# Kernel tuning notes

Hardware: AMD Instinct MI355X
Metric: run time of the kernel (lower is better)

The kernel has to match this reference:

```python
import jax, jax.numpy as jnp
import numpy as np

F = 128; K = 64; SR_CUT = 10.0
NB = 5; NRI = 3; NRA = 2; NRO = 1
N_ATOMS = 10000; N_PAIRS = 320000


def act(x):
    # shifted softplus: softplus(x) - log(2)
    return jax.nn.softplus(x) - jnp.log(2.0).astype(x.dtype)


def residual(x, W1, b1, W2, b2):
    # PhysNet residual: x + dense2(dense1(act(x))) with activation on dense1
    h = act(act(x) @ W1 + b1)
    return x + h @ W2 + b2


def cutoff_fn(D):
    x = D / SR_CUT
    x3 = x * x * x; x4 = x3 * x; x5 = x4 * x
    return jnp.where(x < 1.0, 1.0 - 6.0 * x5 + 15.0 * x4 - 10.0 * x3, 0.0)


def setup_inputs() -> dict:
    key = jax.random.key(0)
    ks = jax.random.split(key, 24)

    def nrm(k, shape, s=0.05):
        return (jax.random.normal(k, shape) * s).astype(jnp.float32)

    inp = {}
    inp["Z"] = jax.random.randint(ks[0], (N_ATOMS,), 1, 95)
    inp["R"] = (jax.random.normal(ks[1], (N_ATOMS, 3)) * 3.0).astype(jnp.float32)
    inp["idx_i"] = jax.random.randint(ks[2], (N_PAIRS,), 0, N_ATOMS)
    inp["idx_j"] = jax.random.randint(ks[3], (N_PAIRS,), 0, N_ATOMS)
    s3 = float(np.sqrt(3.0))
    inp["embeddings"] = jax.random.uniform(ks[4], (95, F), minval=-s3, maxval=s3).astype(jnp.float32)
    inp["rbf_centers"] = jnp.linspace(1.0, float(np.exp(-SR_CUT)), K).astype(jnp.float32)
    width = (0.5 / ((1.0 - float(np.exp(-SR_CUT))) / K)) ** 2
    inp["rbf_widths"] = jnp.full((K,), width, dtype=jnp.float32)
    inp["k2f_W"] = nrm(ks[5], (NB, K, F))
    inp["Wi"] = nrm(ks[6], (NB, F, F)); inp["bi"] = jnp.zeros((NB, F), jnp.float32)
    inp["Wj"] = nrm(ks[7], (NB, F, F)); inp["bj"] = jnp.zeros((NB, F), jnp.float32)
    inp["ri_W1"] = nrm(ks[8], (NB, NRI, F, F)); inp["ri_b1"] = jnp.zeros((NB, NRI, F), jnp.float32)
    inp["ri_W2"] = nrm(ks[9], (NB, NRI, F, F)); inp["ri_b2"] = jnp.zeros((NB, NRI, F), jnp.float32)
    inp["dW"] = nrm(ks[10], (NB, F, F)); inp["db"] = jnp.zeros((NB, F), jnp.float32)
    inp["u"] = jnp.ones((NB, F), jnp.float32)
    inp["ra_W1"] = nrm(ks[11], (NB, NRA, F, F)); inp["ra_b1"] = jnp.zeros((NB, NRA, F), jnp.float32)
    inp["ra_W2"] = nrm(ks[12], (NB, NRA, F, F)); inp["ra_b2"] = jnp.zeros((NB, NRA, F), jnp.float32)
    inp["ro_W1"] = nrm(ks[13], (NB, NRO, F, F)); inp["ro_b1"] = jnp.zeros((NB, NRO, F), jnp.float32)
    inp["ro_W2"] = nrm(ks[14], (NB, NRO, F, F)); inp["ro_b2"] = jnp.zeros((NB, NRO, F), jnp.float32)
    inp["out_W"] = nrm(ks[15], (NB, F, 2))
    inp["Escale"] = jnp.ones((95,), jnp.float32); inp["Eshift"] = jnp.zeros((95,), jnp.float32)
    inp["Qscale"] = jnp.ones((95,), jnp.float32); inp["Qshift"] = jnp.zeros((95,), jnp.float32)
    return inp


def reference(Z, R, idx_i, idx_j, embeddings, rbf_centers, rbf_widths, k2f_W, Wi, bi, Wj, bj,
              ri_W1, ri_b1, ri_W2, ri_b2, dW, db, u, ra_W1, ra_b1, ra_W2, ra_b2,
              ro_W1, ro_b1, ro_W2, ro_b2, out_W, Escale, Eshift, Qscale, Qshift):
    N = R.shape[0]
    # gather-based interatomic distances: gather -> sub -> sumsq -> relu -> sqrt
    dR = R[idx_i] - R[idx_j]                                   # [P,3]
    Dij = jnp.sqrt(jax.nn.relu(jnp.sum(dR * dR, axis=-1)))     # [P]
    # RBF expansion with smooth cutoff
    rbf = cutoff_fn(Dij)[:, None] * jnp.exp(-rbf_widths * (jnp.exp(-Dij)[:, None] - rbf_centers) ** 2)  # [P,K]
    x = embeddings[Z]                                          # [N,F]
    Ea = jnp.zeros((N,), x.dtype)
    Qa = jnp.zeros((N,), x.dtype)
    nhloss = jnp.zeros((), x.dtype)
    last2 = None
    for b in range(NB):
        # --- interaction layer ---
        g = rbf @ k2f_W[b]                                     # [P,F]
        xa = act(x)
        xi = act(xa @ Wi[b] + bi[b])                           # [N,F]
        xj_feat = act(xa @ Wj[b] + bj[b])                      # [N,F]
        msg = g * xj_feat[idx_j]                               # [P,F] gather + modulate
        m = xi + jax.ops.segment_sum(msg, idx_i, num_segments=N)
        for l in range(NRI):
            m = residual(m, ri_W1[b, l], ri_b1[b, l], ri_W2[b, l], ri_b2[b, l])
        m = act(m)
        x = u[b] * x + m @ dW[b] + db[b]
        for l in range(NRA):
            x = residual(x, ra_W1[b, l], ra_b1[b, l], ra_W2[b, l], ra_b2[b, l])
        # --- output block ---
        o = x
        for l in range(NRO):
            o = residual(o, ro_W1[b, l], ro_b1[b, l], ro_W2[b, l], ro_b2[b, l])
        out = act(o) @ out_W[b]                                # [N,2] -> (Ea, Qa)
        Ea = Ea + out[:, 0]
        Qa = Qa + out[:, 1]
        out2 = out * out
        if b > 0:
            nhloss = nhloss + jnp.mean(out2 / (out2 + last2 + 1e-7))
        last2 = out2
    Ea = Escale[Z] * Ea + Eshift[Z]
    Qa = Qscale[Z] * Qa + Qshift[Z]
    return Ea, Qa, Dij, nhloss
```

## Files before the change

### kernel.cpp

```cpp
#include <hip/hip_runtime.h>

typedef __attribute__((ext_vector_type(8))) short bfrag;
typedef __attribute__((ext_vector_type(4))) float ffrag;

__device__ __forceinline__ unsigned short f2b(float f){
  unsigned int u = __float_as_uint(f);
  return (unsigned short)((u + 0x7FFFu + ((u >> 16) & 1u)) >> 16);
}
__device__ __forceinline__ float actf(float v){
  float e = __builtin_amdgcn_exp2f(-fabsf(v)*1.44269504088896341f);
  return fmaxf(v, 0.f) + __builtin_amdgcn_logf(1.f + e)*0.69314718055994531f - 0.69314718055994531f;
}

__global__ __launch_bounds__(256) void k_zero(float* p, int n){
  int i = blockIdx.x*256 + threadIdx.x;
  if (i < n) p[i] = 0.f;
}

__global__ __launch_bounds__(256) void k_dij_count(
    const float* __restrict__ R, const int* __restrict__ idx_i, const int* __restrict__ idx_j,
    float* __restrict__ DijF, float* __restrict__ Dout, int* __restrict__ counts, int P){
  int p = blockIdx.x*256 + threadIdx.x;
  if (p >= P) return;
  int i = idx_i[p], j = idx_j[p];
  float dx = R[i*3+0] - R[j*3+0];
  float dy = R[i*3+1] - R[j*3+1];
  float dz = R[i*3+2] - R[j*3+2];
  float D = sqrtf(fmaxf(dx*dx + dy*dy + dz*dz, 0.f));
  DijF[p] = D;
  Dout[p] = D;
  atomicAdd(&counts[i], 1);
}

__global__ __launch_bounds__(256) void k_scanA(const int* __restrict__ counts,
    int* __restrict__ locEx, int* __restrict__ bsum, int N){
  __shared__ int buf[256];
  int tid = threadIdx.x, idx = blockIdx.x*256 + tid;
  int v = (idx < N) ? counts[idx] : 0;
  buf[tid] = v;
  __syncthreads();
  for (int off = 1; off < 256; off <<= 1){
    int t = (tid >= off) ? buf[tid-off] : 0;
    __syncthreads();
    buf[tid] += t;
    __syncthreads();
  }
  if (idx < N) locEx[idx] = buf[tid] - v;
  if (tid == 255) bsum[blockIdx.x] = buf[255];
}
__global__ __launch_bounds__(64) void k_scanB(int* __restrict__ bsum,
    int* __restrict__ boff, int nb){
  if (threadIdx.x == 0){
    int acc = 0;
    for (int i = 0; i < nb; ++i){ boff[i] = acc; acc += bsum[i]; }
    boff[nb] = acc;
  }
}
__global__ __launch_bounds__(256) void k_scanC(const int* __restrict__ locEx,
    const int* __restrict__ boff, int* __restrict__ starts, int* __restrict__ cursor,
    int N, int nb){
  int idx = blockIdx.x*256 + threadIdx.x;
  if (idx < N){
    int s = locEx[idx] + boff[blockIdx.x];
    starts[idx] = s; cursor[idx] = s;
  }
  if (idx == 0) starts[N] = boff[nb];
}

__global__ __launch_bounds__(256) void k_scatter(const int* __restrict__ idx_i,
    const int* __restrict__ idx_j, const float* __restrict__ DijF,
    int* __restrict__ cursor, int* __restrict__ i_s, int* __restrict__ j_s,
    float* __restrict__ D_s, int P){
  int p = blockIdx.x*256 + threadIdx.x;
  if (p >= P) return;
  int i = idx_i[p];
  int pos = atomicAdd(&cursor[i], 1);
  i_s[pos] = i;
  j_s[pos] = idx_j[p];
  D_s[pos] = DijF[p];
}

__global__ __launch_bounds__(256) void k_rbf(
    const float* __restrict__ D_s, const float* __restrict__ cent, const float* __restrict__ wid,
    unsigned short* __restrict__ rbf_s, int P){
  int gid = blockIdx.x*256 + threadIdx.x;
  if (gid >= P*64) return;
  int t = gid >> 6, k = gid & 63;
  float D = D_s[t];
  float xc = D * 0.1f;
  float cut = 0.f;
  if (xc < 1.f){
    float x3 = xc*xc*xc, x4 = x3*xc, x5 = x4*xc;
    cut = 1.f - 6.f*x5 + 15.f*x4 - 10.f*x3;
  }
  float tt = expf(-D) - cent[k];
  rbf_s[gid] = f2b(cut * expf(-wid[k]*tt*tt));
}

__global__ __launch_bounds__(256) void k_prep(const float* __restrict__ k2f,
    unsigned short* __restrict__ k2fP){
  int gid = blockIdx.x*256 + threadIdx.x;
  if (gid >= 5120) return;
  int l = gid & 63, fr = (gid >> 6) & 15, b = gid >> 10;
  int tile = fr >> 1, kh = fr & 1;
  const float* src = k2f + (size_t)b*64*128;
  int n = tile*16 + (l & 15);
  int kbase = kh*32 + (l >> 4)*8;
  ushort4 o0, o1;
  o0.x = f2b(src[(kbase+0)*128+n]); o0.y = f2b(src[(kbase+1)*128+n]);
  o0.z = f2b(src[(kbase+2)*128+n]); o0.w = f2b(src[(kbase+3)*128+n]);
  o1.x = f2b(src[(kbase+4)*128+n]); o1.y = f2b(src[(kbase+5)*128+n]);
  o1.z = f2b(src[(kbase+6)*128+n]); o1.w = f2b(src[(kbase+7)*128+n]);
  ushort4* dst = (ushort4*)(k2fP + (size_t)gid*8);
  dst[0] = o0; dst[1] = o1;
}

__global__ __launch_bounds__(256) void k_prepAll(
    const float* __restrict__ riW1, const float* __restrict__ riW2,
    const float* __restrict__ dW,   const float* __restrict__ raW1,
    const float* __restrict__ raW2, const float* __restrict__ roW1,
    const float* __restrict__ roW2, const float* __restrict__ Wi,
    const float* __restrict__ Wj,   unsigned short* __restrict__ WBall){
  int gid = blockIdx.x*256 + threadIdx.x;
  if (gid >= 75*2048) return;
  int i = gid >> 11, r = gid & 2047;
  const float* S;
  int slot;
  if (i < 15)      { S = riW1 + (size_t)i*16384;      slot = (i/3)*15 + 2*(i%3); }
  else if (i < 30) { int j=i-15; S = riW2 + (size_t)j*16384; slot = (j/3)*15 + 2*(j%3) + 1; }
  else if (i < 35) { int j=i-30; S = dW   + (size_t)j*16384; slot = j*15 + 6; }
  else if (i < 45) { int j=i-35; S = raW1 + (size_t)j*16384; slot = (j/2)*15 + 7 + 2*(j%2); }
  else if (i < 55) { int j=i-45; S = raW2 + (size_t)j*16384; slot = (j/2)*15 + 8 + 2*(j%2); }
  else if (i < 60) { int j=i-55; S = roW1 + (size_t)j*16384; slot = j*15 + 11; }
  else if (i < 65) { int j=i-60; S = roW2 + (size_t)j*16384; slot = j*15 + 12; }
  else if (i < 70) { int j=i-65; S = Wi   + (size_t)j*16384; slot = ((j==0)?4:(j-1))*15 + 13; }
  else             { int j=i-70; S = Wj   + (size_t)j*16384; slot = ((j==0)?4:(j-1))*15 + 14; }
  int fr = r >> 6, l = r & 63;
  int T = fr >> 2, k0 = fr & 3;
  int n = T*16 + (l & 15);
  int kbase = k0*32 + (l >> 4)*8;
  unsigned short* D = WBall + ((size_t)slot*2048 + r)*8;
  ushort4 o0, o1;
  o0.x=f2b(S[(kbase+0)*128+n]); o0.y=f2b(S[(kbase+1)*128+n]);
  o0.z=f2b(S[(kbase+2)*128+n]); o0.w=f2b(S[(kbase+3)*128+n]);
  o1.x=f2b(S[(kbase+4)*128+n]); o1.y=f2b(S[(kbase+5)*128+n]);
  o1.z=f2b(S[(kbase+6)*128+n]); o1.w=f2b(S[(kbase+7)*128+n]);
  ((ushort4*)D)[0]=o0; ((ushort4*)D)[1]=o1;
}

__global__ __launch_bounds__(256) void k_prepO(const float* __restrict__ outW,
    unsigned short* __restrict__ outWB){
  int gid = blockIdx.x*256 + threadIdx.x;
  if (gid >= 5*256) return;
  int b = gid >> 8, r = gid & 255;
  int l = r & 63;
  int col = l & 15;
  int k0 = r >> 6;
  int kbase = k0*32 + (l >> 4)*8;
  ushort4 o0 = {0,0,0,0}, o1 = {0,0,0,0};
  if (col < 2){
    const float* S = outW + (size_t)b*256;
    o0.x=f2b(S[(kbase+0)*2+col]); o0.y=f2b(S[(kbase+1)*2+col]);
    o0.z=f2b(S[(kbase+2)*2+col]); o0.w=f2b(S[(kbase+3)*2+col]);
    o1.x=f2b(S[(kbase+4)*2+col]); o1.y=f2b(S[(kbase+5)*2+col]);
    o1.z=f2b(S[(kbase+6)*2+col]); o1.w=f2b(S[(kbase+7)*2+col]);
  }
  unsigned short* D = outWB + ((size_t)b*256 + r)*8;
  ((ushort4*)D)[0]=o0; ((ushort4*)D)[1]=o1;
}

__device__ __forceinline__ void mmtile(const unsigned short* tile,
    const unsigned short* __restrict__ WB, int w, int l, ffrag C[4]){
  int m = l & 15, q = l >> 4;
  bfrag A[4];
  #pragma unroll
  for (int k0 = 0; k0 < 4; ++k0)
    A[k0] = *(const bfrag*)(tile + m*136 + k0*32 + q*8);
  #pragma unroll
  for (int tt = 0; tt < 4; ++tt){
    ffrag c = {0.f,0.f,0.f,0.f};
    const bfrag* bp = (const bfrag*)(WB + (((w*4+tt)*4)*64 + l)*8);
    #pragma unroll
    for (int k0 = 0; k0 < 4; ++k0)
      c = __builtin_amdgcn_mfma_f32_16x16x32_bf16(A[k0], bp[k0*64], c, 0, 0, 0);
    C[tt] = c;
  }
}

__device__ __forceinline__ void mmtile2(const unsigned short* tile,
    const unsigned short* __restrict__ WB, int w, int l, ffrag C[2]){
  int m = l & 15, q = l >> 4;
  bfrag A[4];
  #pragma unroll
  for (int k0 = 0; k0 < 4; ++k0)
    A[k0] = *(const bfrag*)(tile + m*136 + k0*32 + q*8);
  #pragma unroll
  for (int tt = 0; tt < 2; ++tt){
    ffrag c = {0.f,0.f,0.f,0.f};
    const bfrag* bp = (const bfrag*)(WB + (((w*2+tt)*4)*64 + l)*8);
    #pragma unroll
    for (int k0 = 0; k0 < 4; ++k0)
      c = __builtin_amdgcn_mfma_f32_16x16x32_bf16(A[k0], bp[k0*64], c, 0, 0, 0);
    C[tt] = c;
  }
}

__global__ __launch_bounds__(128) void k_phase1m(
    const int* __restrict__ Z, const float* __restrict__ emb,
    const unsigned short* __restrict__ WB45,
    const float* __restrict__ bi0, const float* __restrict__ bj0,
    float* __restrict__ x_g, float* __restrict__ m_g, float* __restrict__ xjb_g, int N){
  __shared__ unsigned short tile[16*136];
  int tid = threadIdx.x, w = tid >> 6, l = tid & 63;
  int m = l & 15, q = l >> 4, rbase = blockIdx.x*16;
  #pragma unroll
  for (int r = 0; r < 4; ++r){
    int row = rbase + q*4 + r;
    int z = Z[row];
    #pragma unroll
    for (int tt = 0; tt < 4; ++tt){
      int c = (w*4+tt)*16 + m;
      float v = emb[(size_t)z*128 + c];
      x_g[(size_t)row*128 + c] = v;
      tile[(q*4+r)*136 + c] = f2b(actf(v));
    }
  }
  __syncthreads();
  ffrag C[4];
  mmtile(tile, WB45 + 13*16384, w, l, C);
  #pragma unroll
  for (int tt = 0; tt < 4; ++tt){
    int c = (w*4+tt)*16 + m;
    float bb = bi0[c];
    #pragma unroll
    for (int r = 0; r < 4; ++r)
      m_g[(size_t)(rbase + q*4 + r)*128 + c] = actf(C[tt][r] + bb);
  }
  mmtile(tile, WB45 + 14*16384, w, l, C);
  #pragma unroll
  for (int tt = 0; tt < 4; ++tt){
    int c = (w*4+tt)*16 + m;
    float bb = bj0[c];
    #pragma unroll
    for (int r = 0; r < 4; ++r)
      xjb_g[(size_t)(rbase + q*4 + r)*128 + c] = actf(C[tt][r] + bb);
  }
}

__global__ __launch_bounds__(256) void k_pairmsg2(
    const unsigned short* __restrict__ rbf_s, const unsigned short* __restrict__ k2fP,
    const int* __restrict__ i_s, const int* __restrict__ j_s,
    const float* __restrict__ xj, float* __restrict__ m_g, int P){
  __shared__ float G[4][16*130];
  int tid = threadIdx.x, w = tid >> 6, l = tid & 63;
  float* Gw = &G[w][0];
  bfrag B[8][2];
  #pragma unroll
  for (int t = 0; t < 8; ++t){
    #pragma unroll
    for (int kh = 0; kh < 2; ++kh)
      B[t][kh] = *(const bfrag*)(k2fP + (size_t)((t*2+kh)*64 + l)*8);
  }
  int wstart = (blockIdx.x*4 + w)*128;
  if (wstart >= P) return;
  int row16 = l & 15, quad = l >> 4;
  float a0 = 0.f, a1 = 0.f;
  int iCur = -1;
  #pragma unroll 1
  for (int bt = wstart; bt < wstart + 128; bt += 16){
    int arow = bt + row16;
    bfrag A0 = *(const bfrag*)(rbf_s + (size_t)arow*64 + quad*8);
    bfrag A1 = *(const bfrag*)(rbf_s + (size_t)arow*64 + 32 + quad*8);
    int4 iv[4], jv[4];
    #pragma unroll
    for (int g = 0; g < 4; ++g){
      iv[g] = *(const int4*)(i_s + bt + g*4);
      jv[g] = *(const int4*)(j_s + bt + g*4);
    }
    const int* ip = (const int*)iv;
    const int* jp = (const int*)jv;
    float2 xv[16];
    #pragma unroll
    for (int k = 0; k < 16; ++k)
      xv[k] = *(const float2*)(xj + (size_t)jp[k]*128 + 2*l);
    #pragma unroll
    for (int t = 0; t < 8; ++t){
      ffrag C = {0.f,0.f,0.f,0.f};
      C = __builtin_amdgcn_mfma_f32_16x16x32_bf16(A0, B[t][0], C, 0, 0, 0);
      C = __builtin_amdgcn_mfma_f32_16x16x32_bf16(A1, B[t][1], C, 0, 0, 0);
      #pragma unroll
      for (int r = 0; r < 4; ++r)
        Gw[(quad*4+r)*130 + t*16 + row16] = C[r];
    }
    #pragma unroll
    for (int k = 0; k < 16; ++k){
      int i = ip[k];
      if (i != iCur){
        if (iCur >= 0){
          unsafeAtomicAdd(&m_g[(size_t)iCur*128 + 2*l],     a0);
          unsafeAtomicAdd(&m_g[(size_t)iCur*128 + 2*l + 1], a1);
        }
        iCur = i; a0 = 0.f; a1 = 0.f;
      }
      float g0 = Gw[k*130 + 2*l], g1 = Gw[k*130 + 2*l + 1];
      a0 = fmaf(g0, xv[k].x, a0);
      a1 = fmaf(g1, xv[k].y, a1);
    }
  }
  if (iCur >= 0){
    unsafeAtomicAdd(&m_g[(size_t)iCur*128 + 2*l],     a0);
    unsafeAtomicAdd(&m_g[(size_t)iCur*128 + 2*l + 1], a1);
  }
}

template<int HASNEXT, int NH>
__global__ __launch_bounds__(256) void k_phase2m(
    float* __restrict__ m_g, float* __restrict__ x_g, float* __restrict__ xjb_g,
    const unsigned short* __restrict__ WBb,
    const float* __restrict__ rib1, const float* __restrict__ rib2,
    const float* __restrict__ db, const float* __restrict__ u,
    const float* __restrict__ rab1, const float* __restrict__ rab2,
    const float* __restrict__ rob1, const float* __restrict__ rob2,
    const float* __restrict__ biN, const float* __restrict__ bjN,
    const unsigned short* __restrict__ outWBb,
    float* __restrict__ Ea, float* __restrict__ Qa,
    float* __restrict__ last2, float* __restrict__ nh, int N){
  __shared__ unsigned short tiles[2][16*136];
  __shared__ float biasS[16*128];
  int tid = threadIdx.x, w = tid >> 6, l = tid & 63;
  int m = l & 15, q = l >> 4, rbase = blockIdx.x*16;
  ffrag mC[2], xC[2], C[2];
  int cur = 0;

  if (tid < 128){
    biasS[0*128+tid]  = rib1[tid];
    biasS[1*128+tid]  = rib1[128+tid];
    biasS[2*128+tid]  = rib1[256+tid];
    biasS[3*128+tid]  = rib2[tid];
    biasS[4*128+tid]  = rib2[128+tid];
    biasS[5*128+tid]  = rib2[256+tid];
    biasS[6*128+tid]  = db[tid];
    biasS[7*128+tid]  = u[tid];
    biasS[8*128+tid]  = rab1[tid];
    biasS[9*128+tid]  = rab1[128+tid];
    biasS[10*128+tid] = rab2[tid];
    biasS[11*128+tid] = rab2[128+tid];
    biasS[12*128+tid] = rob1[tid];
    biasS[13*128+tid] = rob2[tid];
    biasS[14*128+tid] = biN[tid];
    biasS[15*128+tid] = bjN[tid];
  }
  #pragma unroll
  for (int tt = 0; tt < 2; ++tt){
    int c = (w*2+tt)*16 + m;
    #pragma unroll
    for (int r = 0; r < 4; ++r){
      float v = m_g[(size_t)(rbase + q*4 + r)*128 + c];
      mC[tt][r] = v;
      tiles[0][(q*4+r)*136 + c] = f2b(actf(v));
    }
  }
  #pragma unroll 1
  for (int li = 0; li < 3; ++li){
    __syncthreads();
    mmtile2(tiles[cur], WBb + (size_t)(2*li)*16384, w, l, C);
    #pragma unroll
    for (int tt = 0; tt < 2; ++tt){
      int c = (w*2+tt)*16 + m;
      float bb = biasS[li*128 + c];
      #pragma unroll
      for (int r = 0; r < 4; ++r)
        tiles[1-cur][(q*4+r)*136 + c] = f2b(actf(C[tt][r] + bb));
    }
    cur ^= 1;
    __syncthreads();
    mmtile2(tiles[cur], WBb + (size_t)(2*li+1)*16384, w, l, C);
    #pragma unroll
    for (int tt = 0; tt < 2; ++tt){
      int c = (w*2+tt)*16 + m;
      float bb = biasS[(3+li)*128 + c];
      #pragma unroll
      for (int r = 0; r < 4; ++r){
        float nv = mC[tt][r] + C[tt][r] + bb;
        mC[tt][r] = nv;
        tiles[1-cur][(q*4+r)*136 + c] = f2b(actf(nv));
      }
    }
    cur ^= 1;
  }
  __syncthreads();
  mmtile2(tiles[cur], WBb + (size_t)6*16384, w, l, C);
  #pragma unroll
  for (int tt = 0; tt < 2; ++tt){
    int c = (w*2+tt)*16 + m;
    float uu = biasS[7*128 + c], bb = biasS[6*128 + c];
    #pragma unroll
    for (int r = 0; r < 4; ++r){
      float xv = x_g[(size_t)(rbase + q*4 + r)*128 + c];
      float nv = uu*xv + C[tt][r] + bb;
      xC[tt][r] = nv;
      tiles[1-cur][(q*4+r)*136 + c] = f2b(actf(nv));
    }
  }
  cur ^= 1;
  #pragma unroll 1
  for (int li = 0; li < 2; ++li){
    __syncthreads();
    mmtile2(tiles[cur], WBb + (size_t)(7+2*li)*16384, w, l, C);
    #pragma unroll
    for (int tt = 0; tt < 2; ++tt){
      int c = (w*2+tt)*16 + m;
      float bb = biasS[(8+li)*128 + c];
      #pragma unroll
      for (int r = 0; r < 4; ++r)
        tiles[1-cur][(q*4+r)*136 + c] = f2b(actf(C[tt][r] + bb));
    }
    cur ^= 1;
    __syncthreads();
    mmtile2(tiles[cur], WBb + (size_t)(8+2*li)*16384, w, l, C);
    #pragma unroll
    for (int tt = 0; tt < 2; ++tt){
      int c = (w*2+tt)*16 + m;
      float bb = biasS[(10+li)*128 + c];
      #pragma unroll
      for (int r = 0; r < 4; ++r){
        float nv = xC[tt][r] + C[tt][r] + bb;
        xC[tt][r] = nv;
        tiles[1-cur][(q*4+r)*136 + c] = f2b(actf(nv));
        if (HASNEXT && li == 1)
          x_g[(size_t)(rbase + q*4 + r)*128 + c] = nv;
      }
    }
    cur ^= 1;
  }
  if (HASNEXT){
    __syncthreads();
    mmtile2(tiles[cur], WBb + (size_t)13*16384, w, l, C);
    #pragma unroll
    for (int tt = 0; tt < 2; ++tt){
      int c = (w*2+tt)*16 + m;
      float bb = biasS[14*128 + c];
      #pragma unroll
      for (int r = 0; r < 4; ++r)
        m_g[(size_t)(rbase + q*4 + r)*128 + c] = actf(C[tt][r] + bb);
    }
    mmtile2(tiles[cur], WBb + (size_t)14*16384, w, l, C);
    #pragma unroll
    for (int tt = 0; tt < 2; ++tt){
      int c = (w*2+tt)*16 + m;
      float bb = biasS[15*128 + c];
      #pragma unroll
      for (int r = 0; r < 4; ++r)
        xjb_g[(size_t)(rbase + q*4 + r)*128 + c] = actf(C[tt][r] + bb);
    }
  }
  __syncthreads();
  mmtile2(tiles[cur], WBb + (size_t)11*16384, w, l, C);
  #pragma unroll
  for (int tt = 0; tt < 2; ++tt){
    int c = (w*2+tt)*16 + m;
    float bb = biasS[12*128 + c];
    #pragma unroll
    for (int r = 0; r < 4; ++r)
      tiles[1-cur][(q*4+r)*136 + c] = f2b(actf(C[tt][r] + bb));
  }
  cur ^= 1;
  __syncthreads();
  mmtile2(tiles[cur], WBb + (size_t)12*16384, w, l, C);
  #pragma unroll
  for (int tt = 0; tt < 2; ++tt){
    int c = (w*2+tt)*16 + m;
    float bb = biasS[13*128 + c];
    #pragma unroll
    for (int r = 0; r < 4; ++r){
      float ov = xC[tt][r] + C[tt][r] + bb;
      tiles[1-cur][(q*4+r)*136 + c] = f2b(actf(ov));
    }
  }
  cur ^= 1;
  __syncthreads();
  if (w == 0){
    bfrag A[4];
    #pragma unroll
    for (int k0 = 0; k0 < 4; ++k0)
      A[k0] = *(const bfrag*)(&tiles[cur][0] + m*136 + k0*32 + q*8);
    ffrag Ch = {0.f,0.f,0.f,0.f};
    #pragma unroll
    for (int k0 = 0; k0 < 4; ++k0){
      bfrag B = *(const bfrag*)(outWBb + (size_t)(k0*64 + l)*8);
      Ch = __builtin_amdgcn_mfma_f32_16x16x32_bf16(A[k0], B, Ch, 0, 0, 0);
    }
    int col = m;
    if (col < 2){
      float tp = 0.f;
      #pragma unroll
      for (int r = 0; r < 4; ++r){
        int row = rbase + q*4 + r;
        float val = Ch[r];
        if (col == 0) Ea[row] += val; else Qa[row] += val;
        float sq = val*val;
        if (NH){
          float lastv = last2[row*2 + col];
          tp += sq/(sq + lastv + 1e-7f);
        }
        last2[row*2 + col] = sq;
      }
      if (NH) unsafeAtomicAdd(nh, tp);
    }
  }
}

__global__ __launch_bounds__(256) void k_final(
    const int* __restrict__ Z, const float* __restrict__ Ea, const float* __restrict__ Qa,
    const float* __restrict__ Es, const float* __restrict__ Eh,
    const float* __restrict__ Qs, const float* __restrict__ Qh,
    const float* __restrict__ nh, float* __restrict__ out, int N, int P){
  int n = blockIdx.x*256 + threadIdx.x;
  if (n < N){
    int z = Z[n];
    out[n]   = Es[z]*Ea[n] + Eh[z];
    out[N+n] = Qs[z]*Qa[n] + Qh[z];
  }
  if (blockIdx.x == 0 && threadIdx.x == 0)
    out[(size_t)2*N + P] = nh[0] / (2.f * (float)N);
}

extern "C" void kernel_launch(void* const* d_in, const int* in_sizes, int n_in,
                              void* d_out, int out_size, void* d_ws, size_t ws_size,
                              hipStream_t stream){
  const int N = in_sizes[0];
  const int P = in_sizes[2];
  const int F = 128;

  const int* Z      = (const int*)d_in[0];
  const float* R    = (const float*)d_in[1];
  const int* idx_i  = (const int*)d_in[2];
  const int* idx_j  = (const int*)d_in[3];
  const float* emb  = (const float*)d_in[4];
  const float* cent = (const float*)d_in[5];
  const float* wid  = (const float*)d_in[6];
  const float* k2f  = (const float*)d_in[7];
  const float* Wi   = (const float*)d_in[8];  const float* bi   = (const float*)d_in[9];
  const float* Wj   = (const float*)d_in[10]; const float* bj   = (const float*)d_in[11];
  const float* riW1 = (const float*)d_in[12]; const float* rib1 = (const float*)d_in[13];
  const float* riW2 = (const float*)d_in[14]; const float* rib2 = (const float*)d_in[15];
  const float* dWp  = (const float*)d_in[16]; const float* dbp  = (const float*)d_in[17];
  const float* u    = (const float*)d_in[18];
  const float* raW1 = (const float*)d_in[19]; const float* rab1 = (const float*)d_in[20];
  const float* raW2 = (const float*)d_in[21]; const float* rab2 = (const float*)d_in[22];
  const float* roW1 = (const float*)d_in[23]; const float* rob1 = (const float*)d_in[24];
  const float* roW2 = (const float*)d_in[25]; const float* rob2 = (const float*)d_in[26];
  const float* outW = (const float*)d_in[27];
  const float* Es   = (const float*)d_in[28]; const float* Eh   = (const float*)d_in[29];
  const float* Qs   = (const float*)d_in[30]; const float* Qh   = (const float*)d_in[31];

  char* ws = (char*)d_ws;
  size_t off = 0;
  float* DijF  = (float*)(ws + off); off += (size_t)P*4;
  float* D_s   = (float*)(ws + off); off += (size_t)P*4;
  int*   i_s   = (int*)  (ws + off); off += (size_t)P*4;
  int*   j_s   = (int*)  (ws + off); off += (size_t)P*4;
  unsigned short* rbf_s = (unsigned short*)(ws + off); off += (size_t)P*64*2;
  unsigned short* k2fP  = (unsigned short*)(ws + off); off += (size_t)5*16*64*8*2;
  unsigned short* WBall = (unsigned short*)(ws + off); off += (size_t)75*16384*2;
  unsigned short* outWB = (unsigned short*)(ws + off); off += (size_t)5*2048*2;
  float* x     = (float*)(ws + off); off += (size_t)N*F*4;
  float* xjb   = (float*)(ws + off); off += (size_t)N*F*4;
  float* m     = (float*)(ws + off); off += (size_t)N*F*4;
  float* last2 = (float*)(ws + off); off += (size_t)N*2*4;
  float* Ea    = (float*)(ws + off); off += (size_t)N*4;
  float* Qa    = (float*)(ws + off); off += (size_t)N*4;
  float* nh    = (float*)(ws + off); off += 256;
  int*   counts= (int*)  (ws + off); off += (size_t)N*4;
  int*   starts= (int*)  (ws + off); off += (size_t)(N+1)*4;
  int*   cursor= (int*)  (ws + off); off += (size_t)N*4;
  int*   locEx = (int*)  (ws + off); off += (size_t)N*4;
  int*   bsum  = (int*)  (ws + off); off += 64*4;
  int*   boff  = (int*)  (ws + off); off += 68*4;

  float* outF = (float*)d_out;
  float* Dout = outF + (size_t)2*N;

  const int nb = (N + 255)/256;
  const int nzero = 3*N + 64;
  k_zero<<<dim3((nzero+255)/256), dim3(256), 0, stream>>>(Ea, nzero);
  k_dij_count<<<dim3((P+255)/256), dim3(256), 0, stream>>>(R, idx_i, idx_j, DijF, Dout, counts, P);
  k_scanA<<<dim3(nb), dim3(256), 0, stream>>>(counts, locEx, bsum, N);
  k_scanB<<<dim3(1), dim3(64), 0, stream>>>(bsum, boff, nb);
  k_scanC<<<dim3(nb), dim3(256), 0, stream>>>(locEx, boff, starts, cursor, N, nb);
  k_scatter<<<dim3((P+255)/256), dim3(256), 0, stream>>>(idx_i, idx_j, DijF, cursor, i_s, j_s, D_s, P);
  k_rbf<<<dim3((P*64+255)/256), dim3(256), 0, stream>>>(D_s, cent, wid, rbf_s, P);
  k_prep<<<dim3(20), dim3(256), 0, stream>>>(k2f, k2fP);
  k_prepAll<<<dim3((75*2048+255)/256), dim3(256), 0, stream>>>(riW1, riW2, dWp, raW1, raW2,
                                                               roW1, roW2, Wi, Wj, WBall);
  k_prepO<<<dim3(5), dim3(256), 0, stream>>>(outW, outWB);

  const int G16 = (N + 15)/16;
  k_phase1m<<<dim3(G16), dim3(128), 0, stream>>>(Z, emb, WBall + (size_t)4*15*16384,
                                                 bi, bj, x, m, xjb, N);

  const int pmg = (P + 511)/512;
  for (int b = 0; b < 5; ++b){
    k_pairmsg2<<<dim3(pmg), dim3(256), 0, stream>>>(rbf_s, k2fP + (size_t)b*16*64*8,
                                                    i_s, j_s, xjb, m, P);
    const unsigned short* WBb = WBall + (size_t)b*15*16384;
    const float* a_rib1 = rib1 + (size_t)b*3*F;
    const float* a_rib2 = rib2 + (size_t)b*3*F;
    const float* a_db   = dbp  + (size_t)b*F;
    const float* a_u    = u    + (size_t)b*F;
    const float* a_rab1 = rab1 + (size_t)b*2*F;
    const float* a_rab2 = rab2 + (size_t)b*2*F;
    const float* a_rob1 = rob1 + (size_t)b*F;
    const float* a_rob2 = rob2 + (size_t)b*F;
    int bn = (b < 4) ? (b+1) : 0;
    const float* a_biN = bi + (size_t)bn*F;
    const float* a_bjN = bj + (size_t)bn*F;
    const unsigned short* oWB = outWB + (size_t)b*2048;
    if (b == 0){
      k_phase2m<1,0><<<dim3(G16), dim3(256), 0, stream>>>(m, x, xjb, WBb,
        a_rib1, a_rib2, a_db, a_u, a_rab1, a_rab2, a_rob1, a_rob2,
        a_biN, a_bjN, oWB, Ea, Qa, last2, nh, N);
    } else if (b < 4){
      k_phase2m<1,1><<<dim3(G16), dim3(256), 0, stream>>>(m, x, xjb, WBb,
        a_rib1, a_rib2, a_db, a_u, a_rab1, a_rab2, a_rob1, a_rob2,
        a_biN, a_bjN, oWB, Ea, Qa, last2, nh, N);
    } else {
      k_phase2m<0,1><<<dim3(G16), dim3(256), 0, stream>>>(m, x, xjb, WBb,
        a_rib1, a_rib2, a_db, a_u, a_rab1, a_rab2, a_rob1, a_rob2,
        a_biN, a_bjN, oWB, Ea, Qa, last2, nh, N);
    }
  }
  k_final<<<dim3((N+255)/256), dim3(256), 0, stream>>>(Z, Ea, Qa, Es, Eh, Qs, Qh, nh, outF, N, P);
}
```

Measured before the change: 520.8 us.

## Software-pipeline weight fragment and rbf/index loads in pair and node kernels

Measured after the change: 518.9 us (median of 2 runs). About the same (-0.4%).

```diff
diff --git a/kernel.cpp b/kernel.cpp
--- a/kernel.cpp
+++ b/kernel.cpp
@@ -187,8 +187,16 @@
   }
 }
 
-__device__ __forceinline__ void mmtile2(const unsigned short* tile,
-    const unsigned short* __restrict__ WB, int w, int l, ffrag C[2]){
+__device__ __forceinline__ void loadB8(const unsigned short* __restrict__ WB,
+    int w, int l, bfrag* B){
+  #pragma unroll
+  for (int tt = 0; tt < 2; ++tt)
+    #pragma unroll
+    for (int k0 = 0; k0 < 4; ++k0)
+      B[tt*4+k0] = *(const bfrag*)(WB + ((size_t)((((w*2+tt)*4)+k0)*64 + l))*8);
+}
+__device__ __forceinline__ void mmB(const unsigned short* tile, const bfrag* B,
+    int l, ffrag C[2]){
   int m = l & 15, q = l >> 4;
   bfrag A[4];
   #pragma unroll
@@ -197,10 +205,9 @@
   #pragma unroll
   for (int tt = 0; tt < 2; ++tt){
     ffrag c = {0.f,0.f,0.f,0.f};
-    const bfrag* bp = (const bfrag*)(WB + (((w*2+tt)*4)*64 + l)*8);
     #pragma unroll
     for (int k0 = 0; k0 < 4; ++k0)
-      c = __builtin_amdgcn_mfma_f32_16x16x32_bf16(A[k0], bp[k0*64], c, 0, 0, 0);
+      c = __builtin_amdgcn_mfma_f32_16x16x32_bf16(A[k0], B[tt*4+k0], c, 0, 0, 0);
     C[tt] = c;
   }
 }
@@ -254,29 +261,29 @@
   __shared__ float G[4][16*130];
   int tid = threadIdx.x, w = tid >> 6, l = tid & 63;
   float* Gw = &G[w][0];
-  bfrag B[8][2];
+  bfrag B[16];
   #pragma unroll
   for (int t = 0; t < 8; ++t){
     #pragma unroll
     for (int kh = 0; kh < 2; ++kh)
-      B[t][kh] = *(const bfrag*)(k2fP + (size_t)((t*2+kh)*64 + l)*8);
+      B[t*2+kh] = *(const bfrag*)(k2fP + (size_t)((t*2+kh)*64 + l)*8);
   }
   int wstart = (blockIdx.x*4 + w)*128;
   if (wstart >= P) return;
   int row16 = l & 15, quad = l >> 4;
   float a0 = 0.f, a1 = 0.f;
   int iCur = -1;
+  bfrag A0 = *(const bfrag*)(rbf_s + (size_t)(wstart + row16)*64 + quad*8);
+  bfrag A1 = *(const bfrag*)(rbf_s + (size_t)(wstart + row16)*64 + 32 + quad*8);
+  int4 iv[4], jv[4];
+  #pragma unroll
+  for (int g = 0; g < 4; ++g){
+    iv[g] = *(const int4*)(i_s + wstart + g*4);
+    jv[g] = *(const int4*)(j_s + wstart + g*4);
+  }
   #pragma unroll 1
-  for (int bt = wstart; bt < wstart + 128; bt += 16){
-    int arow = bt + row16;
-    bfrag A0 = *(const bfrag*)(rbf_s + (size_t)arow*64 + quad*8);
-    bfrag A1 = *(const bfrag*)(rbf_s + (size_t)arow*64 + 32 + quad*8);
-    int4 iv[4], jv[4];
-    #pragma unroll
-    for (int g = 0; g < 4; ++g){
-      iv[g] = *(const int4*)(i_s + bt + g*4);
-      jv[g] = *(const int4*)(j_s + bt + g*4);
-    }
+  for (int bi2 = 0; bi2 < 8; ++bi2){
+    int bt = wstart + bi2*16;
     const int* ip = (const int*)iv;
     const int* jp = (const int*)jv;
     float2 xv[16];
@@ -286,11 +293,23 @@
     #pragma unroll
     for (int t = 0; t < 8; ++t){
       ffrag C = {0.f,0.f,0.f,0.f};
-      C = __builtin_amdgcn_mfma_f32_16x16x32_bf16(A0, B[t][0], C, 0, 0, 0);
-      C = __builtin_amdgcn_mfma_f32_16x16x32_bf16(A1, B[t][1], C, 0, 0, 0);
+      C = __builtin_amdgcn_mfma_f32_16x16x32_bf16(A0, B[t*2],   C, 0, 0, 0);
+      C = __builtin_amdgcn_mfma_f32_16x16x32_bf16(A1, B[t*2+1], C, 0, 0, 0);
       #pragma unroll
       for (int r = 0; r < 4; ++r)
         Gw[(quad*4+r)*130 + t*16 + row16] = C[r];
+    }
+    bfrag nA0, nA1;
+    int4 niv[4], njv[4];
+    if (bi2 < 7){
+      int btn = bt + 16;
+      nA0 = *(const bfrag*)(rbf_s + (size_t)(btn + row16)*64 + quad*8);
+      nA1 = *(const bfrag*)(rbf_s + (size_t)(btn + row16)*64 + 32 + quad*8);
+      #pragma unroll
+      for (int g = 0; g < 4; ++g){
+        niv[g] = *(const int4*)(i_s + btn + g*4);
+        njv[g] = *(const int4*)(j_s + btn + g*4);
+      }
     }
     #pragma unroll
     for (int k = 0; k < 16; ++k){
@@ -305,6 +324,11 @@
       float g0 = Gw[k*130 + 2*l], g1 = Gw[k*130 + 2*l + 1];
       a0 = fmaf(g0, xv[k].x, a0);
       a1 = fmaf(g1, xv[k].y, a1);
+    }
+    if (bi2 < 7){
+      A0 = nA0; A1 = nA1;
+      #pragma unroll
+      for (int g = 0; g < 4; ++g){ iv[g] = niv[g]; jv[g] = njv[g]; }
     }
   }
   if (iCur >= 0){
@@ -331,6 +355,11 @@
   int m = l & 15, q = l >> 4, rbase = blockIdx.x*16;
   ffrag mC[2], xC[2], C[2];
   int cur = 0;
+  const int nst = HASNEXT ? 15 : 13;
+  const int slotSeq[15] = {0,1,2,3,4,5,6,7,8,9,10,
+                           HASNEXT?13:11, HASNEXT?14:12, 11, 12};
+  bfrag Bb[2][8];
+  loadB8(WBb + (size_t)slotSeq[0]*16384, w, l, Bb[0]);
 
   if (tid < 128){
     biasS[0*128+tid]  = rib1[tid];
@@ -350,6 +379,14 @@
     biasS[14*128+tid] = biN[tid];
     biasS[15*128+tid] = bjN[tid];
   }
+  float xrow[2][4];
+  #pragma unroll
+  for (int tt = 0; tt < 2; ++tt){
+    int c = (w*2+tt)*16 + m;
+    #pragma unroll
+    for (int r = 0; r < 4; ++r)
+      xrow[tt][r] = x_g[(size_t)(rbase + q*4 + r)*128 + c];
+  }
   #pragma unroll
   for (int tt = 0; tt < 2; ++tt){
     int c = (w*2+tt)*16 + m;
@@ -360,124 +397,95 @@
       tiles[0][(q*4+r)*136 + c] = f2b(actf(v));
     }
   }
-  #pragma unroll 1
-  for (int li = 0; li < 3; ++li){
+  #pragma unroll
+  for (int s = 0; s < nst; ++s){
     __syncthreads();
-    mmtile2(tiles[cur], WBb + (size_t)(2*li)*16384, w, l, C);
-    #pragma unroll
-    for (int tt = 0; tt < 2; ++tt){
-      int c = (w*2+tt)*16 + m;
-      float bb = biasS[li*128 + c];
-      #pragma unroll
-      for (int r = 0; r < 4; ++r)
-        tiles[1-cur][(q*4+r)*136 + c] = f2b(actf(C[tt][r] + bb));
-    }
-    cur ^= 1;
-    __syncthreads();
-    mmtile2(tiles[cur], WBb + (size_t)(2*li+1)*16384, w, l, C);
-    #pragma unroll
-    for (int tt = 0; tt < 2; ++tt){
-      int c = (w*2+tt)*16 + m;
-      float bb = biasS[(3+li)*128 + c];
-      #pragma unroll
-      for (int r = 0; r < 4; ++r){
-        float nv = mC[tt][r] + C[tt][r] + bb;
-        mC[tt][r] = nv;
-        tiles[1-cur][(q*4+r)*136 + c] = f2b(actf(nv));
-      }
-    }
-    cur ^= 1;
-  }
-  __syncthreads();
-  mmtile2(tiles[cur], WBb + (size_t)6*16384, w, l, C);
-  #pragma unroll
-  for (int tt = 0; tt < 2; ++tt){
-    int c = (w*2+tt)*16 + m;
-    float uu = biasS[7*128 + c], bb = biasS[6*128 + c];
-    #pragma unroll
-    for (int r = 0; r < 4; ++r){
-      float xv = x_g[(size_t)(rbase + q*4 + r)*128 + c];
-      float nv = uu*xv + C[tt][r] + bb;
-      xC[tt][r] = nv;
-      tiles[1-cur][(q*4+r)*136 + c] = f2b(actf(nv));
-    }
-  }
-  cur ^= 1;
-  #pragma unroll 1
-  for (int li = 0; li < 2; ++li){
-    __syncthreads();
-    mmtile2(tiles[cur], WBb + (size_t)(7+2*li)*16384, w, l, C);
-    #pragma unroll
-    for (int tt = 0; tt < 2; ++tt){
-      int c = (w*2+tt)*16 + m;
-      float bb = biasS[(8+li)*128 + c];
-      #pragma unroll
-      for (int r = 0; r < 4; ++r)
-        tiles[1-cur][(q*4+r)*136 + c] = f2b(actf(C[tt][r] + bb));
-    }
-    cur ^= 1;
-    __syncthreads();
-    mmtile2(tiles[cur], WBb + (size_t)(8+2*li)*16384, w, l, C);
-    #pragma unroll
-    for (int tt = 0; tt < 2; ++tt){
-      int c = (w*2+tt)*16 + m;
-      float bb = biasS[(10+li)*128 + c];
-      #pragma unroll
-      for (int r = 0; r < 4; ++r){
-        float nv = xC[tt][r] + C[tt][r] + bb;
-        xC[tt][r] = nv;
-        tiles[1-cur][(q*4+r)*136 + c] = f2b(actf(nv));
-        if (HASNEXT && li == 1)
-          x_g[(size_t)(rbase + q*4 + r)*128 + c] = nv;
-      }
-    }
-    cur ^= 1;
-  }
-  if (HASNEXT){
-    __syncthreads();
-    mmtile2(tiles[cur], WBb + (size_t)13*16384, w, l, C);
-    #pragma unroll
-    for (int tt = 0; tt < 2; ++tt){
-      int c = (w*2+tt)*16 + m;
-      float bb = biasS[14*128 + c];
-      #pragma unroll
-      for (int r = 0; r < 4; ++r)
-        m_g[(size_t)(rbase + q*4 + r)*128 + c] = actf(C[tt][r] + bb);
-    }
-    mmtile2(tiles[cur], WBb + (size_t)14*16384, w, l, C);
-    #pragma unroll
-    for (int tt = 0; tt < 2; ++tt){
-      int c = (w*2+tt)*16 + m;
-      float bb = biasS[15*128 + c];
-      #pragma unroll
-      for (int r = 0; r < 4; ++r)
-        xjb_g[(size_t)(rbase + q*4 + r)*128 + c] = actf(C[tt][r] + bb);
-    }
-  }
-  __syncthreads();
-  mmtile2(tiles[cur], WBb + (size_t)11*16384, w, l, C);
-  #pragma unroll
-  for (int tt = 0; tt < 2; ++tt){
-    int c = (w*2+tt)*16 + m;
-    float bb = biasS[12*128 + c];
-    #pragma unroll
-    for (int r = 0; r < 4; ++r)
-      tiles[1-cur][(q*4+r)*136 + c] = f2b(actf(C[tt][r] + bb));
-  }
-  cur ^= 1;
-  __syncthreads();
-  mmtile2(tiles[cur], WBb + (size_t)12*16384, w, l, C);
-  #pragma unroll
-  for (int tt = 0; tt < 2; ++tt){
-    int c = (w*2+tt)*16 + m;
-    float bb = biasS[13*128 + c];
-    #pragma unroll
-    for (int r = 0; r < 4; ++r){
-      float ov = xC[tt][r] + C[tt][r] + bb;
-      tiles[1-cur][(q*4+r)*136 + c] = f2b(actf(ov));
-    }
-  }
-  cur ^= 1;
+    if (s+1 < nst) loadB8(WBb + (size_t)slotSeq[s+1]*16384, w, l, Bb[(s+1)&1]);
+    mmB(tiles[cur], Bb[s&1], l, C);
+    if (HASNEXT && s == 11){
+      #pragma unroll
+      for (int tt = 0; tt < 2; ++tt){
+        int c = (w*2+tt)*16 + m;
+        float bb = biasS[14*128 + c];
+        #pragma unroll
+        for (int r = 0; r < 4; ++r)
+          m_g[(size_t)(rbase + q*4 + r)*128 + c] = actf(C[tt][r] + bb);
+      }
+    } else if (HASNEXT && s == 12){
+      #pragma unroll
+      for (int tt = 0; tt < 2; ++tt){
+        int c = (w*2+tt)*16 + m;
+        float bb = biasS[15*128 + c];
+        #pragma unroll
+        for (int r = 0; r < 4; ++r)
+          xjb_g[(size_t)(rbase + q*4 + r)*128 + c] = actf(C[tt][r] + bb);
+      }
+    } else if (s == 6){
+      #pragma unroll
+      for (int tt = 0; tt < 2; ++tt){
+        int c = (w*2+tt)*16 + m;
+        float uu = biasS[7*128 + c], bb = biasS[6*128 + c];
+        #pragma unroll
+        for (int r = 0; r < 4; ++r){
+          float nv = uu*xrow[tt][r] + C[tt][r] + bb;
+          xC[tt][r] = nv;
+          tiles[1-cur][(q*4+r)*136 + c] = f2b(actf(nv));
+        }
+      }
+      cur ^= 1;
+    } else if (s == 1 || s == 3 || s == 5){
+      #pragma unroll
+      for (int tt = 0; tt < 2; ++tt){
+        int c = (w*2+tt)*16 + m;
+        float bb = biasS[(3 + (s>>1))*128 + c];
+        #pragma unroll
+        for (int r = 0; r < 4; ++r){
+          float nv = mC[tt][r] + C[tt][r] + bb;
+          mC[tt][r] = nv;
+          tiles[1-cur][(q*4+r)*136 + c] = f2b(actf(nv));
+        }
+      }
+      cur ^= 1;
+    } else if (s == 8 || s == 10){
+      #pragma unroll
+      for (int tt = 0; tt < 2; ++tt){
+        int c = (w*2+tt)*16 + m;
+        float bb = biasS[(10 + ((s-8)>>1))*128 + c];
+        #pragma unroll
+        for (int r = 0; r < 4; ++r){
+          float nv = xC[tt][r] + C[tt][r] + bb;
+          xC[tt][r] = nv;
+          tiles[1-cur][(q*4+r)*136 + c] = f2b(actf(nv));
+          if (HASNEXT && s == 10)
+            x_g[(size_t)(rbase + q*4 + r)*128 + c] = nv;
+        }
+      }
+      cur ^= 1;
+    } else if ((HASNEXT && s == 14) || (!HASNEXT && s == 12)){
+      #pragma unroll
+      for (int tt = 0; tt < 2; ++tt){
+        int c = (w*2+tt)*16 + m;
+        float bb = biasS[13*128 + c];
+        #pragma unroll
+        for (int r = 0; r < 4; ++r){
+          float ov = xC[tt][r] + C[tt][r] + bb;
+          tiles[1-cur][(q*4+r)*136 + c] = f2b(actf(ov));
+        }
+      }
+      cur ^= 1;
+    } else {
+      int bidx = (s==0)?0:(s==2)?1:(s==4)?2:(s==7)?8:(s==9)?9:12;
+      #pragma unroll
+      for (int tt = 0; tt < 2; ++tt){
+        int c = (w*2+tt)*16 + m;
+        float bb = biasS[bidx*128 + c];
+        #pragma unroll
+        for (int r = 0; r < 4; ++r)
+          tiles[1-cur][(q*4+r)*136 + c] = f2b(actf(C[tt][r] + bb));
+      }
+      cur ^= 1;
+    }
+  }
   __syncthreads();
   if (w == 0){
     bfrag A[4];
```
